# Kernel tuning notes

Hardware: AMD Instinct MI355X
Metric: run time of the kernel (lower is better)

Reference implementation:

```python
import jax, jax.numpy as jnp
import numpy as np

EPS = 1e-5


def _bn(h, gamma, beta):
    # BatchNorm1d in training mode: batch statistics over node dim
    mu = h.mean(axis=0)
    var = h.var(axis=0)
    return gamma * (h - mu) * jax.lax.rsqrt(var + EPS) + beta


def _rgcn_layer(x, src, dst, etype, W, Wloop, b, n_dst):
    # Relation-specific gather-transform-scatter (DGL RelGraphConv, sum agg,
    # self-loop + bias, no regularizer).
    x_src = x[src]                                   # [E, in] gather
    num_rels = W.shape[0]
    m = jnp.zeros((x_src.shape[0], W.shape[2]), x.dtype)
    for r in range(num_rels):                        # small fixed relation count
        m = m + jnp.where((etype == r)[:, None], x_src @ W[r], 0.0)
    agg = jax.ops.segment_sum(m, dst, num_segments=n_dst)  # scatter-add to dst
    # DGL block convention: dst nodes are the prefix of src nodes
    return agg + x[:n_dst] @ Wloop + b


def setup_inputs() -> dict:
    key = jax.random.key(0)
    ks = jax.random.split(key, 16)
    N_SRC, N_DST0, N_DST1 = 200000, 50000, 10000
    E0, E1, R, H, C = 800000, 160000, 5, 256, 153
    s = 1.0 / np.sqrt(H)
    inp = {
        "x": jax.random.normal(ks[0], (N_SRC, H), jnp.float32),
        "src0": jax.random.randint(ks[1], (E0,), 0, N_SRC, jnp.int32),
        "dst0": jax.random.randint(ks[2], (E0,), 0, N_DST0, jnp.int32),
        "etype0": jax.random.randint(ks[3], (E0,), 0, R, jnp.int32),
        "src1": jax.random.randint(ks[4], (E1,), 0, N_DST0, jnp.int32),
        "dst1": jax.random.randint(ks[5], (E1,), 0, N_DST1, jnp.int32),
        "etype1": jax.random.randint(ks[6], (E1,), 0, R, jnp.int32),
        "n_dst0": N_DST0,
        "n_dst1": N_DST1,
        "W0": jax.random.normal(ks[7], (R, H, H), jnp.float32) * s,
        "Wl0": jax.random.normal(ks[8], (H, H), jnp.float32) * s,
        "b0": jnp.zeros((H,), jnp.float32),
        "g0": jnp.ones((H,), jnp.float32),
        "be0": jnp.zeros((H,), jnp.float32),
        "W1": jax.random.normal(ks[9], (R, H, H), jnp.float32) * s,
        "Wl1": jax.random.normal(ks[10], (H, H), jnp.float32) * s,
        "b1": jnp.zeros((H,), jnp.float32),
        "g1": jnp.ones((H,), jnp.float32),
        "be1": jnp.zeros((H,), jnp.float32),
        "Wm1": jax.random.normal(ks[11], (H, H), jnp.float32) * s,
        "bm1": jnp.zeros((H,), jnp.float32),
        "gm": jnp.ones((H,), jnp.float32),
        "bem": jnp.zeros((H,), jnp.float32),
        "Wm2": jax.random.normal(ks[12], (H, C), jnp.float32) * s,
        "bm2": jnp.zeros((C,), jnp.float32),
    }
    return inp


def reference(x, src0, dst0, etype0, src1, dst1, etype1, n_dst0, n_dst1,
              W0, Wl0, b0, g0, be0, W1, Wl1, b1, g1, be1,
              Wm1, bm1, gm, bem, Wm2, bm2):
    # layer 0
    h = _rgcn_layer(x, src0, dst0, etype0, W0, Wl0, b0, n_dst0)
    h = jax.nn.elu(_bn(h, g0, be0))
    # layer 1
    h = _rgcn_layer(h, src1, dst1, etype1, W1, Wl1, b1, n_dst1)
    h = jax.nn.elu(_bn(h, g1, be1))
    # MLP head (dropout is identity in eval)
    h = jax.nn.relu(_bn(h @ Wm1 + bm1, gm, bem))
    return h @ Wm2 + bm2
```

## Files before the change

### kernel.cpp

```cpp
#include <hip/hip_runtime.h>
#include <hip/hip_bf16.h>


#define HD   256
#define EPS  1e-5f
#define NREL 5
#define ND0  50000
#define ND1  10000
#define BK   64
#define PAD  8

typedef unsigned short ushort_t;
using f32x4  = __attribute__((ext_vector_type(4))) float;
using short8 = __attribute__((ext_vector_type(8))) short;

__device__ __forceinline__ ushort_t f2b(float f) {
    union { float f; unsigned u; } x; x.f = f;
    unsigned r = x.u + 0x7FFF + ((x.u >> 16) & 1);
    return (ushort_t)(r >> 16);
}
__device__ __forceinline__ float b2f(ushort_t h) {
    union { unsigned u; float f; } x; x.u = ((unsigned)h) << 16;
    return x.f;
}

struct WconvArgs {
    const float* src[14];
    ushort_t*    dst[14];
    int          N[14];
};
__global__ void wconv_all_kernel(WconvArgs a) {
    int mat = blockIdx.x >> 8;
    int id = (blockIdx.x & 255) * 256 + threadIdx.x;
    int n = id >> 8, k = id & 255;
    int N = a.N[mat];
    float v = (n < N) ? a.src[mat][(size_t)k * N + n] : 0.f;
    a.dst[mat][id] = f2b(v);
}

__global__ void xconv_kernel(const float* __restrict__ x, ushort_t* __restrict__ xb,
                             int n4) {
    int id = blockIdx.x * 256 + threadIdx.x;
    if (id >= n4) return;
    float4 v = ((const float4*)x)[id];
    ushort4 o; o.x = f2b(v.x); o.y = f2b(v.y); o.z = f2b(v.z); o.w = f2b(v.w);
    ((ushort4*)xb)[id] = o;
}

__global__ void count2_kernel(const int* __restrict__ d0, const int* __restrict__ e0, int E0,
                              const int* __restrict__ d1, const int* __restrict__ e1, int E1,
                              int* __restrict__ cnt, int* __restrict__ pos) {
    int e = blockIdx.x * 256 + threadIdx.x;
    if (e < E0) {
        pos[e] = atomicAdd(&cnt[e0[e] * ND0 + d0[e]], 1);
    } else if (e < E0 + E1) {
        int i = e - E0;
        pos[e] = atomicAdd(&cnt[NREL * ND0 + e1[i] * ND1 + d1[i]], 1);
    }
}

__global__ void scan_block_kernel(const int* __restrict__ in, int* __restrict__ out,
                                  int* __restrict__ bsum, int nb) {
    __shared__ int ts[256];
    int tid = threadIdx.x;
    int base = blockIdx.x * 1024 + tid * 4;
    int v0 = (base + 0 < nb) ? in[base + 0] : 0;
    int v1 = (base + 1 < nb) ? in[base + 1] : 0;
    int v2 = (base + 2 < nb) ? in[base + 2] : 0;
    int v3 = (base + 3 < nb) ? in[base + 3] : 0;
    int tsum = v0 + v1 + v2 + v3;
    ts[tid] = tsum;
    __syncthreads();
    for (int d = 1; d < 256; d <<= 1) {
        int t = (tid >= d) ? ts[tid - d] : 0;
        __syncthreads();
        ts[tid] += t;
        __syncthreads();
    }
    int excl = ts[tid] - tsum;
    if (base + 0 < nb) out[base + 0] = excl;
    if (base + 1 < nb) out[base + 1] = excl + v0;
    if (base + 2 < nb) out[base + 2] = excl + v0 + v1;
    if (base + 3 < nb) out[base + 3] = excl + v0 + v1 + v2;
    if (tid == 255 && bsum) bsum[blockIdx.x] = ts[255];
}

__global__ void scan_add_kernel(int* __restrict__ out, const int* __restrict__ bsum, int nb) {
    int i = blockIdx.x * 256 + threadIdx.x;
    if (i < nb) out[i] += bsum[i >> 10];
}

__global__ void fill2_kernel(const int* __restrict__ s0, const int* __restrict__ d0,
                             const int* __restrict__ e0, int E0,
                             const int* __restrict__ s1, const int* __restrict__ d1,
                             const int* __restrict__ e1, int E1,
                             const int* __restrict__ pos, const int* __restrict__ off,
                             int* __restrict__ ssrc) {
    int e = blockIdx.x * 256 + threadIdx.x;
    if (e < E0) {
        ssrc[off[e0[e] * ND0 + d0[e]] + pos[e]] = s0[e];
    } else if (e < E0 + E1) {
        int i = e - E0;
        ssrc[off[NREL * ND0 + e1[i] * ND1 + d1[i]] + pos[e]] = s1[i];
    }
}

__global__ void gather_kernel(const ushort_t* __restrict__ feat, const int* __restrict__ ssrc,
                              const int* __restrict__ cnt, const int* __restrict__ off,
                              int nbuckets, ushort_t* __restrict__ out,
                              const float* __restrict__ sc, const float* __restrict__ sh) {
    int wave = (blockIdx.x * 256 + threadIdx.x) >> 6;
    int lane = threadIdx.x & 63;
    if (wave >= nbuckets) return;
    int deg = cnt[wave], s = off[wave];
    float4 scv = {0, 0, 0, 0}, shv = {0, 0, 0, 0};
    if (sc) { scv = ((const float4*)sc)[lane]; shv = ((const float4*)sh)[lane]; }
    float a0 = 0, a1 = 0, a2 = 0, a3 = 0;
    if (sc) {
        for (int j = 0; j < deg; j++) {
            ushort4 v = ((const ushort4*)(feat + (size_t)ssrc[s + j] * HD))[lane];
            float f0 = fmaf(b2f(v.x), scv.x, shv.x);
            float f1 = fmaf(b2f(v.y), scv.y, shv.y);
            float f2 = fmaf(b2f(v.z), scv.z, shv.z);
            float f3 = fmaf(b2f(v.w), scv.w, shv.w);
            a0 += f0 > 0.f ? f0 : expm1f(f0);
            a1 += f1 > 0.f ? f1 : expm1f(f1);
            a2 += f2 > 0.f ? f2 : expm1f(f2);
            a3 += f3 > 0.f ? f3 : expm1f(f3);
        }
    } else {
        int j = 0;
        for (; j + 2 <= deg; j += 2) {
            int r0 = ssrc[s + j], r1 = ssrc[s + j + 1];
            ushort4 v0 = ((const ushort4*)(feat + (size_t)r0 * HD))[lane];
            ushort4 v1 = ((const ushort4*)(feat + (size_t)r1 * HD))[lane];
            a0 += b2f(v0.x) + b2f(v1.x); a1 += b2f(v0.y) + b2f(v1.y);
            a2 += b2f(v0.z) + b2f(v1.z); a3 += b2f(v0.w) + b2f(v1.w);
        }
        if (j < deg) {
            ushort4 v = ((const ushort4*)(feat + (size_t)ssrc[s + j] * HD))[lane];
            a0 += b2f(v.x); a1 += b2f(v.y); a2 += b2f(v.z); a3 += b2f(v.w);
        }
    }
    ushort4 o; o.x = f2b(a0); o.y = f2b(a1); o.z = f2b(a2); o.w = f2b(a3);
    ((ushort4*)(out + (size_t)wave * HD))[lane] = o;
}

__global__ void bnprep_kernel(const float* __restrict__ sums, const float* __restrict__ g,
                              const float* __restrict__ be, float invM,
                              float* __restrict__ sc, float* __restrict__ sh) {
    int c = threadIdx.x;
    float mu = sums[c] * invM;
    float var = sums[HD + c] * invM - mu * mu;
    float s = g[c] * rsqrtf(var + EPS);
    sc[c] = s; sh[c] = be[c] - mu * s;
}

struct Seg {
    const ushort_t* A;
    const ushort_t* B;
    const float* sc;
    const float* sh;
    int act;
};
struct GemmArgs {
    Seg seg[6];
    int nseg;
    const float* bias;
    float* stats;
    ushort_t* Cb;
    float* Cf;
    int M, N;
};

template <int BM>
__launch_bounds__(256)
__global__ void gemm_mfma_kernel(GemmArgs g) {
    constexpr int F = BM / 32;
    __shared__ __align__(16) ushort_t As[BM][BK + PAD];
    __shared__ __align__(16) ushort_t Bs[BM][BK + PAD];
    int tid = threadIdx.x;
    int wave = tid >> 6, lane = tid & 63;
    int rq = lane >> 4, ci = lane & 15;
    int wm = (wave >> 1) * (BM / 2), wn = (wave & 1) * (BM / 2);
    int bm = blockIdx.y * BM, bn = blockIdx.x * BM;
    f32x4 acc[F][F] = {};
    int K = g.nseg * HD;

    for (int kk = 0; kk < K; kk += BK) {
        int si = kk >> 8;
        int kl = kk & 255;
        const ushort_t* Ap = g.seg[si].A;
        const ushort_t* Bp = g.seg[si].B;
        const float* sc = g.seg[si].sc;
#pragma unroll
        for (int it = 0; it < BM / 32; it++) {
            int idx = tid + it * 256;
            int row = idx >> 3, c8 = idx & 7;
            uint4 v = *(const uint4*)(Ap + (size_t)(bm + row) * HD + kl + c8 * 8);
            if (sc) {
                const float* sh = g.seg[si].sh;
                int act = g.seg[si].act;
                ushort_t* u = (ushort_t*)&v;
                int kb = kl + c8 * 8;
#pragma unroll
                for (int j = 0; j < 8; j++) {
                    float f = fmaf(b2f(u[j]), sc[kb + j], sh[kb + j]);
                    f = (act == 2) ? fmaxf(f, 0.f) : (f > 0.f ? f : expm1f(f));
                    u[j] = f2b(f);
                }
            }
            *(uint4*)&As[row][c8 * 8] = v;
        }
#pragma unroll
        for (int it = 0; it < BM / 32; it++) {
            int idx = tid + it * 256;
            int row = idx >> 3, c8 = idx & 7;
            *(uint4*)&Bs[row][c8 * 8] =
                *(const uint4*)(Bp + (size_t)(bn + row) * HD + kl + c8 * 8);
        }
        __syncthreads();
#pragma unroll
        for (int ks = 0; ks < BK; ks += 32) {
            int kq = ks + rq * 8;
            short8 a[F], b[F];
#pragma unroll
            for (int mi = 0; mi < F; mi++)
                a[mi] = *(const short8*)&As[wm + mi * 16 + ci][kq];
#pragma unroll
            for (int ni = 0; ni < F; ni++)
                b[ni] = *(const short8*)&Bs[wn + ni * 16 + ci][kq];
#pragma unroll
            for (int mi = 0; mi < F; mi++)
#pragma unroll
                for (int ni = 0; ni < F; ni++)
                    acc[mi][ni] = __builtin_amdgcn_mfma_f32_16x16x32_bf16(
                        a[mi], b[ni], acc[mi][ni], 0, 0, 0);
        }
        __syncthreads();
    }

#pragma unroll
    for (int ni = 0; ni < F; ni++) {
        int col = bn + wn + ni * 16 + ci;
        float bv = (col < g.N) ? g.bias[col] : 0.f;
#pragma unroll
        for (int mi = 0; mi < F; mi++)
#pragma unroll
            for (int reg = 0; reg < 4; reg++) acc[mi][ni][reg] += bv;
    }
    if (g.stats) {
#pragma unroll
        for (int ni = 0; ni < F; ni++) {
            float s = 0.f, s2 = 0.f;
#pragma unroll
            for (int mi = 0; mi < F; mi++)
#pragma unroll
                for (int reg = 0; reg < 4; reg++) {
                    int row = bm + wm + mi * 16 + rq * 4 + reg;
                    if (row < g.M) { float v = acc[mi][ni][reg]; s += v; s2 += v * v; }
                }
            s  += __shfl_xor(s, 16);  s  += __shfl_xor(s, 32);
            s2 += __shfl_xor(s2, 16); s2 += __shfl_xor(s2, 32);
            if (rq == 0) {
                int col = bn + wn + ni * 16 + ci;
                atomicAdd(&g.stats[col], s);
                atomicAdd(&g.stats[HD + col], s2);
            }
        }
    }
#pragma unroll
    for (int mi = 0; mi < F; mi++)
#pragma unroll
        for (int ni = 0; ni < F; ni++)
#pragma unroll
            for (int reg = 0; reg < 4; reg++) {
                int row = bm + wm + mi * 16 + rq * 4 + reg;
                int col = bn + wn + ni * 16 + ci;
                if (row < g.M && col < g.N) {
                    float v = acc[mi][ni][reg];
                    if (g.Cb) g.Cb[(size_t)row * HD + col] = f2b(v);
                    else      g.Cf[(size_t)row * g.N + col] = v;
                }
            }
}

extern "C" void kernel_launch(void* const* d_in, const int* in_sizes, int n_in,
                              void* d_out, int out_size, void* d_ws, size_t ws_size,
                              hipStream_t stream) {
    const float* x   = (const float*)d_in[0];
    const int* src0  = (const int*)d_in[1];
    const int* dst0  = (const int*)d_in[2];
    const int* et0   = (const int*)d_in[3];
    const int* src1  = (const int*)d_in[4];
    const int* dst1  = (const int*)d_in[5];
    const int* et1   = (const int*)d_in[6];
    const float* W0  = (const float*)d_in[9];
    const float* Wl0 = (const float*)d_in[10];
    const float* b0  = (const float*)d_in[11];
    const float* g0  = (const float*)d_in[12];
    const float* be0 = (const float*)d_in[13];
    const float* W1  = (const float*)d_in[14];
    const float* Wl1 = (const float*)d_in[15];
    const float* b1  = (const float*)d_in[16];
    const float* g1  = (const float*)d_in[17];
    const float* be1 = (const float*)d_in[18];
    const float* Wm1 = (const float*)d_in[19];
    const float* bm1 = (const float*)d_in[20];
    const float* gm  = (const float*)d_in[21];
    const float* bem = (const float*)d_in[22];
    const float* Wm2 = (const float*)d_in[23];
    const float* bm2 = (const float*)d_in[24];

    const int E0 = in_sizes[1];
    const int E1 = in_sizes[4];
    const int NOUT = in_sizes[24];
    const int NSRC = in_sizes[0] / HD;
    const int NBKT = NREL * ND0 + NREL * ND1;

    char* p = (char*)d_ws;
    ushort_t* Wt = (ushort_t*)p;  p += (size_t)14 * 65536 * 2;
    float* st    = (float*)p;     p += 1536 * 4;
    float* bnp   = (float*)p;     p += 6 * 256 * 4;
    int* cnt     = (int*)p;       p += (size_t)NBKT * 4;
    int* off     = (int*)p;       p += (size_t)NBKT * 4;
    int* bsum    = (int*)p;       p += 1024 * 4;
    int* pos     = (int*)p;       p += (size_t)(E0 + E1) * 4;
    int* ssrc    = (int*)p;       p += (size_t)(E0 + E1) * 4;
    ushort_t* xb  = (ushort_t*)p; p += (size_t)NSRC * HD * 2;
    ushort_t* S0  = (ushort_t*)p; p += (size_t)(NREL * ND0 + 128) * HD * 2;
    ushort_t* S1  = (ushort_t*)p; p += (size_t)(NREL * ND1 + 128) * HD * 2;
    ushort_t* h0b = (ushort_t*)p; p += (size_t)(ND0 + 128) * HD * 2;
    ushort_t* h1b = (ushort_t*)p; p += (size_t)(ND1 + 128) * HD * 2;
    ushort_t* mb  = (ushort_t*)p; p += (size_t)(ND1 + 128) * HD * 2;

    float* st0 = st, *st1 = st + 512, *stm = st + 1024;
    float* sc0 = bnp, *sh0 = bnp + 256, *sc1 = bnp + 512, *sh1 = bnp + 768;
    float* scm = bnp + 1024, *shm = bnp + 1280;

    ushort_t* W0t  = Wt;
    ushort_t* Wl0t = Wt + 5 * 65536;
    ushort_t* W1t  = Wt + 6 * 65536;
    ushort_t* Wl1t = Wt + 11 * 65536;
    ushort_t* Wm1t = Wt + 12 * 65536;
    ushort_t* Wm2t = Wt + 13 * 65536;

    {
        WconvArgs wa;
        for (int r = 0; r < NREL; r++) { wa.src[r] = W0 + (size_t)r * 65536; wa.dst[r] = W0t + (size_t)r * 65536; wa.N[r] = 256; }
        wa.src[5] = Wl0; wa.dst[5] = Wl0t; wa.N[5] = 256;
        for (int r = 0; r < NREL; r++) { wa.src[6 + r] = W1 + (size_t)r * 65536; wa.dst[6 + r] = W1t + (size_t)r * 65536; wa.N[6 + r] = 256; }
        wa.src[11] = Wl1; wa.dst[11] = Wl1t; wa.N[11] = 256;
        wa.src[12] = Wm1; wa.dst[12] = Wm1t; wa.N[12] = 256;
        wa.src[13] = Wm2; wa.dst[13] = Wm2t; wa.N[13] = NOUT;
        wconv_all_kernel<<<14 * 256, 256, 0, stream>>>(wa);
    }
    xconv_kernel<<<(NSRC * 64 + 255) / 256, 256, 0, stream>>>(x, xb, NSRC * 64);
    hipMemsetAsync(st, 0, 1536 * sizeof(float), stream);
    hipMemsetAsync(cnt, 0, (size_t)NBKT * sizeof(int), stream);

    int ET = E0 + E1;
    count2_kernel<<<(ET + 255) / 256, 256, 0, stream>>>(dst0, et0, E0, dst1, et1, E1, cnt, pos);
    int nsb = (NBKT + 1023) / 1024;
    scan_block_kernel<<<nsb, 256, 0, stream>>>(cnt, off, bsum, NBKT);
    scan_block_kernel<<<1, 256, 0, stream>>>(bsum, bsum, nullptr, nsb);
    scan_add_kernel<<<(NBKT + 255) / 256, 256, 0, stream>>>(off, bsum, NBKT);
    fill2_kernel<<<(ET + 255) / 256, 256, 0, stream>>>(src0, dst0, et0, E0, src1, dst1, et1, E1, pos, off, ssrc);

    gather_kernel<<<(NREL * ND0 * 64) / 256, 256, 0, stream>>>(
        xb, ssrc, cnt, off, NREL * ND0, S0, nullptr, nullptr);
    {
        GemmArgs ga = {};
        for (int s = 0; s < NREL; s++)
            ga.seg[s] = { S0 + (size_t)s * ND0 * HD, W0t + (size_t)s * 65536, nullptr, nullptr, 0 };
        ga.seg[5] = { xb, Wl0t, nullptr, nullptr, 0 };
        ga.nseg = 6; ga.bias = b0; ga.stats = st0;
        ga.Cb = h0b; ga.Cf = nullptr; ga.M = ND0; ga.N = HD;
        gemm_mfma_kernel<128><<<dim3(2, (ND0 + 127) / 128), 256, 0, stream>>>(ga);
    }
    bnprep_kernel<<<1, 256, 0, stream>>>(st0, g0, be0, 1.f / ND0, sc0, sh0);

    gather_kernel<<<(NREL * ND1 * 64) / 256, 256, 0, stream>>>(
        h0b, ssrc, cnt + NREL * ND0, off + NREL * ND0, NREL * ND1, S1, sc0, sh0);
    {
        GemmArgs ga = {};
        for (int s = 0; s < NREL; s++)
            ga.seg[s] = { S1 + (size_t)s * ND1 * HD, W1t + (size_t)s * 65536, nullptr, nullptr, 0 };
        ga.seg[5] = { h0b, Wl1t, sc0, sh0, 1 };
        ga.nseg = 6; ga.bias = b1; ga.stats = st1;
        ga.Cb = h1b; ga.Cf = nullptr; ga.M = ND1; ga.N = HD;
        gemm_mfma_kernel<64><<<dim3(4, (ND1 + 63) / 64), 256, 0, stream>>>(ga);
    }
    bnprep_kernel<<<1, 256, 0, stream>>>(st1, g1, be1, 1.f / ND1, sc1, sh1);

    {
        GemmArgs ga = {};
        ga.seg[0] = { h1b, Wm1t, sc1, sh1, 1 };
        ga.nseg = 1; ga.bias = bm1; ga.stats = stm;
        ga.Cb = mb; ga.Cf = nullptr; ga.M = ND1; ga.N = HD;
        gemm_mfma_kernel<64><<<dim3(4, (ND1 + 63) / 64), 256, 0, stream>>>(ga);
    }
    bnprep_kernel<<<1, 256, 0, stream>>>(stm, gm, bem, 1.f / ND1, scm, shm);
    {
        GemmArgs ga = {};
        ga.seg[0] = { mb, Wm2t, scm, shm, 2 };
        ga.nseg = 1; ga.bias = bm2; ga.stats = nullptr;
        ga.Cb = nullptr; ga.Cf = (float*)d_out; ga.M = ND1; ga.N = NOUT;
        gemm_mfma_kernel<64><<<dim3((NOUT + 63) / 64, (ND1 + 63) / 64), 256, 0, stream>>>(ga);
    }
}
```

Measured before the change: 820.7 us.

## Prefetch GEMM tiles into registers, swizzle LDS layout, unroll gather by four

The GEMM kernel now loads the next K tile from global memory into registers while MFMAs run on the current LDS tile, then writes it to shared memory after the compute. The padded shared-memory layout is replaced with an XOR swizzle to avoid bank conflicts at lower LDS usage, and launch bounds request two blocks per CU. The unnormalized gather loop is unrolled to four rows in flight to expose more memory parallelism. The register prefetch adds register pressure, which could clash with the occupancy hint.

```diff
diff --git a/kernel.cpp b/kernel.cpp
--- a/kernel.cpp
+++ b/kernel.cpp
@@ -8,7 +8,6 @@
 #define ND0  50000
 #define ND1  10000
 #define BK   64
-#define PAD  8
 
 typedef unsigned short ushort_t;
 using f32x4  = __attribute__((ext_vector_type(4))) float;
@@ -113,10 +112,10 @@
     int lane = threadIdx.x & 63;
     if (wave >= nbuckets) return;
     int deg = cnt[wave], s = off[wave];
-    float4 scv = {0, 0, 0, 0}, shv = {0, 0, 0, 0};
-    if (sc) { scv = ((const float4*)sc)[lane]; shv = ((const float4*)sh)[lane]; }
     float a0 = 0, a1 = 0, a2 = 0, a3 = 0;
     if (sc) {
+        float4 scv = ((const float4*)sc)[lane];
+        float4 shv = ((const float4*)sh)[lane];
         for (int j = 0; j < deg; j++) {
             ushort4 v = ((const ushort4*)(feat + (size_t)ssrc[s + j] * HD))[lane];
             float f0 = fmaf(b2f(v.x), scv.x, shv.x);
@@ -130,14 +129,19 @@
         }
     } else {
         int j = 0;
-        for (; j + 2 <= deg; j += 2) {
+        for (; j + 4 <= deg; j += 4) {
             int r0 = ssrc[s + j], r1 = ssrc[s + j + 1];
+            int r2 = ssrc[s + j + 2], r3 = ssrc[s + j + 3];
             ushort4 v0 = ((const ushort4*)(feat + (size_t)r0 * HD))[lane];
             ushort4 v1 = ((const ushort4*)(feat + (size_t)r1 * HD))[lane];
-            a0 += b2f(v0.x) + b2f(v1.x); a1 += b2f(v0.y) + b2f(v1.y);
-            a2 += b2f(v0.z) + b2f(v1.z); a3 += b2f(v0.w) + b2f(v1.w);
-        }
-        if (j < deg) {
+            ushort4 v2 = ((const ushort4*)(feat + (size_t)r2 * HD))[lane];
+            ushort4 v3 = ((const ushort4*)(feat + (size_t)r3 * HD))[lane];
+            a0 += (b2f(v0.x) + b2f(v1.x)) + (b2f(v2.x) + b2f(v3.x));
+            a1 += (b2f(v0.y) + b2f(v1.y)) + (b2f(v2.y) + b2f(v3.y));
+            a2 += (b2f(v0.z) + b2f(v1.z)) + (b2f(v2.z) + b2f(v3.z));
+            a3 += (b2f(v0.w) + b2f(v1.w)) + (b2f(v2.w) + b2f(v3.w));
+        }
+        for (; j < deg; j++) {
             ushort4 v = ((const ushort4*)(feat + (size_t)ssrc[s + j] * HD))[lane];
             a0 += b2f(v.x); a1 += b2f(v.y); a2 += b2f(v.z); a3 += b2f(v.w);
         }
@@ -174,11 +178,12 @@
 };
 
 template <int BM>
-__launch_bounds__(256)
+__launch_bounds__(256, 2)
 __global__ void gemm_mfma_kernel(GemmArgs g) {
-    constexpr int F = BM / 32;
-    __shared__ __align__(16) ushort_t As[BM][BK + PAD];
-    __shared__ __align__(16) ushort_t Bs[BM][BK + PAD];
+    constexpr int F  = BM / 32;
+    constexpr int IT = BM / 32;
+    __shared__ __align__(16) ushort_t As[BM * BK];
+    __shared__ __align__(16) ushort_t Bs[BM * BK];
     int tid = threadIdx.x;
     int wave = tid >> 6, lane = tid & 63;
     int rq = lane >> 4, ci = lane & 15;
@@ -187,22 +192,36 @@
     f32x4 acc[F][F] = {};
     int K = g.nseg * HD;
 
-    for (int kk = 0; kk < K; kk += BK) {
-        int si = kk >> 8;
-        int kl = kk & 255;
+    uint4 ra[IT], rb[IT];
+    int srow[IT], soct[IT];
+#pragma unroll
+    for (int it = 0; it < IT; it++) {
+        int idx = tid + it * 256;
+        srow[it] = idx >> 3;
+        soct[it] = idx & 7;
+    }
+
+    auto load_tile = [&](int kk) {
+        int si = kk >> 8, kl = kk & 255;
         const ushort_t* Ap = g.seg[si].A;
         const ushort_t* Bp = g.seg[si].B;
+#pragma unroll
+        for (int it = 0; it < IT; it++) {
+            ra[it] = *(const uint4*)(Ap + (size_t)(bm + srow[it]) * HD + kl + soct[it] * 8);
+            rb[it] = *(const uint4*)(Bp + (size_t)(bn + srow[it]) * HD + kl + soct[it] * 8);
+        }
+    };
+    auto store_tile = [&](int kk) {
+        int si = kk >> 8, kl = kk & 255;
         const float* sc = g.seg[si].sc;
 #pragma unroll
-        for (int it = 0; it < BM / 32; it++) {
-            int idx = tid + it * 256;
-            int row = idx >> 3, c8 = idx & 7;
-            uint4 v = *(const uint4*)(Ap + (size_t)(bm + row) * HD + kl + c8 * 8);
+        for (int it = 0; it < IT; it++) {
+            uint4 v = ra[it];
             if (sc) {
                 const float* sh = g.seg[si].sh;
                 int act = g.seg[si].act;
                 ushort_t* u = (ushort_t*)&v;
-                int kb = kl + c8 * 8;
+                int kb = kl + soct[it] * 8;
 #pragma unroll
                 for (int j = 0; j < 8; j++) {
                     float f = fmaf(b2f(u[j]), sc[kb + j], sh[kb + j]);
@@ -210,26 +229,31 @@
                     u[j] = f2b(f);
                 }
             }
-            *(uint4*)&As[row][c8 * 8] = v;
-        }
-#pragma unroll
-        for (int it = 0; it < BM / 32; it++) {
-            int idx = tid + it * 256;
-            int row = idx >> 3, c8 = idx & 7;
-            *(uint4*)&Bs[row][c8 * 8] =
-                *(const uint4*)(Bp + (size_t)(bn + row) * HD + kl + c8 * 8);
-        }
+            int sw = soct[it] ^ (srow[it] & 7);
+            *(uint4*)&As[srow[it] * BK + sw * 8] = v;
+            *(uint4*)&Bs[srow[it] * BK + sw * 8] = rb[it];
+        }
+    };
+
+    load_tile(0);
+    store_tile(0);
+    for (int kk = 0; kk < K; kk += BK) {
         __syncthreads();
+        if (kk + BK < K) load_tile(kk + BK);
 #pragma unroll
         for (int ks = 0; ks < BK; ks += 32) {
-            int kq = ks + rq * 8;
+            int O = (ks >> 3) + rq;
             short8 a[F], b[F];
 #pragma unroll
-            for (int mi = 0; mi < F; mi++)
-                a[mi] = *(const short8*)&As[wm + mi * 16 + ci][kq];
-#pragma unroll
-            for (int ni = 0; ni < F; ni++)
-                b[ni] = *(const short8*)&Bs[wn + ni * 16 + ci][kq];
+            for (int mi = 0; mi < F; mi++) {
+                int R = wm + mi * 16 + ci;
+                a[mi] = *(const short8*)&As[R * BK + ((O ^ (R & 7)) * 8)];
+            }
+#pragma unroll
+            for (int ni = 0; ni < F; ni++) {
+                int R = wn + ni * 16 + ci;
+                b[ni] = *(const short8*)&Bs[R * BK + ((O ^ (R & 7)) * 8)];
+            }
 #pragma unroll
             for (int mi = 0; mi < F; mi++)
 #pragma unroll
@@ -238,6 +262,7 @@
                         a[mi], b[ni], acc[mi][ni], 0, 0, 0);
         }
         __syncthreads();
+        if (kk + BK < K) store_tile(kk + BK);
     }
 
 #pragma unroll
```

After: 832.3 us. No clear change (+1.4%).

## Replace LDS-tiled GEMM with direct global-to-register MFMA loads; unroll gather by four

Applied to the files above, without the earlier changes.

The GEMM no longer stages A and B tiles through shared memory with barriers. Each wave instead loads its MFMA fragments straight from global memory into registers and relies on cache for reuse between waves, with an occupancy hint of 3 blocks per CU. The intent is to remove LDS traffic and __syncthreads stalls, at the risk of redundant global and L2 loads across waves and less coalesced access. Separately, the unnormalised gather loop is unrolled from two to four rows per iteration to keep more loads in flight.

```diff
diff --git a/kernel.cpp b/kernel.cpp
--- a/kernel.cpp
+++ b/kernel.cpp
@@ -7,8 +7,6 @@
 #define NREL 5
 #define ND0  50000
 #define ND1  10000
-#define BK   64
-#define PAD  8
 
 typedef unsigned short ushort_t;
 using f32x4  = __attribute__((ext_vector_type(4))) float;
@@ -113,10 +111,10 @@
     int lane = threadIdx.x & 63;
     if (wave >= nbuckets) return;
     int deg = cnt[wave], s = off[wave];
-    float4 scv = {0, 0, 0, 0}, shv = {0, 0, 0, 0};
-    if (sc) { scv = ((const float4*)sc)[lane]; shv = ((const float4*)sh)[lane]; }
     float a0 = 0, a1 = 0, a2 = 0, a3 = 0;
     if (sc) {
+        float4 scv = ((const float4*)sc)[lane];
+        float4 shv = ((const float4*)sh)[lane];
         for (int j = 0; j < deg; j++) {
             ushort4 v = ((const ushort4*)(feat + (size_t)ssrc[s + j] * HD))[lane];
             float f0 = fmaf(b2f(v.x), scv.x, shv.x);
@@ -130,14 +128,19 @@
         }
     } else {
         int j = 0;
-        for (; j + 2 <= deg; j += 2) {
+        for (; j + 4 <= deg; j += 4) {
             int r0 = ssrc[s + j], r1 = ssrc[s + j + 1];
+            int r2 = ssrc[s + j + 2], r3 = ssrc[s + j + 3];
             ushort4 v0 = ((const ushort4*)(feat + (size_t)r0 * HD))[lane];
             ushort4 v1 = ((const ushort4*)(feat + (size_t)r1 * HD))[lane];
-            a0 += b2f(v0.x) + b2f(v1.x); a1 += b2f(v0.y) + b2f(v1.y);
-            a2 += b2f(v0.z) + b2f(v1.z); a3 += b2f(v0.w) + b2f(v1.w);
+            ushort4 v2 = ((const ushort4*)(feat + (size_t)r2 * HD))[lane];
+            ushort4 v3 = ((const ushort4*)(feat + (size_t)r3 * HD))[lane];
+            a0 += (b2f(v0.x) + b2f(v1.x)) + (b2f(v2.x) + b2f(v3.x));
+            a1 += (b2f(v0.y) + b2f(v1.y)) + (b2f(v2.y) + b2f(v3.y));
+            a2 += (b2f(v0.z) + b2f(v1.z)) + (b2f(v2.z) + b2f(v3.z));
+            a3 += (b2f(v0.w) + b2f(v1.w)) + (b2f(v2.w) + b2f(v3.w));
         }
-        if (j < deg) {
+        for (; j < deg; j++) {
             ushort4 v = ((const ushort4*)(feat + (size_t)ssrc[s + j] * HD))[lane];
             a0 += b2f(v.x); a1 += b2f(v.y); a2 += b2f(v.z); a3 += b2f(v.w);
         }
@@ -173,71 +176,76 @@
     int M, N;
 };
 
-template <int BM>
-__launch_bounds__(256)
-__global__ void gemm_mfma_kernel(GemmArgs g) {
-    constexpr int F = BM / 32;
-    __shared__ __align__(16) ushort_t As[BM][BK + PAD];
-    __shared__ __align__(16) ushort_t Bs[BM][BK + PAD];
+template <int F>
+__launch_bounds__(256, 3)
+__global__ void gemm_direct_kernel(GemmArgs g) {
+    constexpr int WT = F * 16;
     int tid = threadIdx.x;
     int wave = tid >> 6, lane = tid & 63;
     int rq = lane >> 4, ci = lane & 15;
-    int wm = (wave >> 1) * (BM / 2), wn = (wave & 1) * (BM / 2);
-    int bm = blockIdx.y * BM, bn = blockIdx.x * BM;
+    int wm = (wave >> 1) * WT, wn = (wave & 1) * WT;
+    int bm = blockIdx.y * (2 * WT), bn = blockIdx.x * (2 * WT);
     f32x4 acc[F][F] = {};
-    int K = g.nseg * HD;
-
-    for (int kk = 0; kk < K; kk += BK) {
-        int si = kk >> 8;
-        int kl = kk & 255;
-        const ushort_t* Ap = g.seg[si].A;
-        const ushort_t* Bp = g.seg[si].B;
-        const float* sc = g.seg[si].sc;
-#pragma unroll
-        for (int it = 0; it < BM / 32; it++) {
-            int idx = tid + it * 256;
-            int row = idx >> 3, c8 = idx & 7;
-            uint4 v = *(const uint4*)(Ap + (size_t)(bm + row) * HD + kl + c8 * 8);
-            if (sc) {
-                const float* sh = g.seg[si].sh;
-                int act = g.seg[si].act;
-                ushort_t* u = (ushort_t*)&v;
-                int kb = kl + c8 * 8;
-#pragma unroll
-                for (int j = 0; j < 8; j++) {
-                    float f = fmaf(b2f(u[j]), sc[kb + j], sh[kb + j]);
-                    f = (act == 2) ? fmaxf(f, 0.f) : (f > 0.f ? f : expm1f(f));
-                    u[j] = f2b(f);
+
+    size_t aoff[F], boff[F];
+#pragma unroll
+    for (int mi = 0; mi < F; mi++)
+        aoff[mi] = (size_t)(bm + wm + mi * 16 + ci) * HD + rq * 8;
+#pragma unroll
+    for (int ni = 0; ni < F; ni++)
+        boff[ni] = (size_t)(bn + wn + ni * 16 + ci) * HD + rq * 8;
+
+    for (int s = 0; s < g.nseg; s++) {
+        const ushort_t* Ap = g.seg[s].A;
+        const ushort_t* Bp = g.seg[s].B;
+        const float* sc = g.seg[s].sc;
+        if (sc) {
+            const float* sh = g.seg[s].sh;
+            int act = g.seg[s].act;
+#pragma unroll 2
+            for (int kl = 0; kl < 256; kl += 32) {
+                short8 a[F], b[F];
+#pragma unroll
+                for (int mi = 0; mi < F; mi++) {
+                    short8 v = *(const short8*)(Ap + aoff[mi] + kl);
+                    ushort_t* u = (ushort_t*)&v;
+                    int kb = kl + rq * 8;
+#pragma unroll
+                    for (int j = 0; j < 8; j++) {
+                        float f = fmaf(b2f(u[j]), sc[kb + j], sh[kb + j]);
+                        f = (act == 2) ? fmaxf(f, 0.f) : (f > 0.f ? f : expm1f(f));
+                        u[j] = f2b(f);
+                    }
+                    a[mi] = v;
                 }
+#pragma unroll
+                for (int ni = 0; ni < F; ni++)
+                    b[ni] = *(const short8*)(Bp + boff[ni] + kl);
+#pragma unroll
+                for (int mi = 0; mi < F; mi++)
+#pragma unroll
+                    for (int ni = 0; ni < F; ni++)
+                        acc[mi][ni] = __builtin_amdgcn_mfma_f32_16x16x32_bf16(
+                            a[mi], b[ni], acc[mi][ni], 0, 0, 0);
             }
-            *(uint4*)&As[row][c8 * 8] = v;
+        } else {
+#pragma unroll 2
+            for (int kl = 0; kl < 256; kl += 32) {
+                short8 a[F], b[F];
+#pragma unroll
+                for (int mi = 0; mi < F; mi++)
+                    a[mi] = *(const short8*)(Ap + aoff[mi] + kl);
+#pragma unroll
+                for (int ni = 0; ni < F; ni++)
+                    b[ni] = *(const short8*)(Bp + boff[ni] + kl);
+#pragma unroll
+                for (int mi = 0; mi < F; mi++)
+#pragma unroll
+                    for (int ni = 0; ni < F; ni++)
+                        acc[mi][ni] = __builtin_amdgcn_mfma_f32_16x16x32_bf16(
+                            a[mi], b[ni], acc[mi][ni], 0, 0, 0);
+            }
         }
-#pragma unroll
-        for (int it = 0; it < BM / 32; it++) {
-            int idx = tid + it * 256;
-            int row = idx >> 3, c8 = idx & 7;
-            *(uint4*)&Bs[row][c8 * 8] =
-                *(const uint4*)(Bp + (size_t)(bn + row) * HD + kl + c8 * 8);
-        }
-        __syncthreads();
-#pragma unroll
-        for (int ks = 0; ks < BK; ks += 32) {
-            int kq = ks + rq * 8;
-            short8 a[F], b[F];
-#pragma unroll
-            for (int mi = 0; mi < F; mi++)
-                a[mi] = *(const short8*)&As[wm + mi * 16 + ci][kq];
-#pragma unroll
-            for (int ni = 0; ni < F; ni++)
-                b[ni] = *(const short8*)&Bs[wn + ni * 16 + ci][kq];
-#pragma unroll
-            for (int mi = 0; mi < F; mi++)
-#pragma unroll
-                for (int ni = 0; ni < F; ni++)
-                    acc[mi][ni] = __builtin_amdgcn_mfma_f32_16x16x32_bf16(
-                        a[mi], b[ni], acc[mi][ni], 0, 0, 0);
-        }
-        __syncthreads();
     }
 
 #pragma unroll
@@ -376,7 +384,7 @@
         ga.seg[5] = { xb, Wl0t, nullptr, nullptr, 0 };
         ga.nseg = 6; ga.bias = b0; ga.stats = st0;
         ga.Cb = h0b; ga.Cf = nullptr; ga.M = ND0; ga.N = HD;
-        gemm_mfma_kernel<128><<<dim3(2, (ND0 + 127) / 128), 256, 0, stream>>>(ga);
+        gemm_direct_kernel<4><<<dim3(2, (ND0 + 127) / 128), 256, 0, stream>>>(ga);
     }
     bnprep_kernel<<<1, 256, 0, stream>>>(st0, g0, be0, 1.f / ND0, sc0, sh0);
 
@@ -389,7 +397,7 @@
         ga.seg[5] = { h0b, Wl1t, sc0, sh0, 1 };
         ga.nseg = 6; ga.bias = b1; ga.stats = st1;
         ga.Cb = h1b; ga.Cf = nullptr; ga.M = ND1; ga.N = HD;
-        gemm_mfma_kernel<64><<<dim3(4, (ND1 + 63) / 64), 256, 0, stream>>>(ga);
+        gemm_direct_kernel<2><<<dim3(4, (ND1 + 63) / 64), 256, 0, stream>>>(ga);
     }
     bnprep_kernel<<<1, 256, 0, stream>>>(st1, g1, be1, 1.f / ND1, sc1, sh1);
 
@@ -398,7 +406,7 @@
         ga.seg[0] = { h1b, Wm1t, sc1, sh1, 1 };
         ga.nseg = 1; ga.bias = bm1; ga.stats = stm;
         ga.Cb = mb; ga.Cf = nullptr; ga.M = ND1; ga.N = HD;
-        gemm_mfma_kernel<64><<<dim3(4, (ND1 + 63) / 64), 256, 0, stream>>>(ga);
+        gemm_direct_kernel<2><<<dim3(4, (ND1 + 63) / 64), 256, 0, stream>>>(ga);
     }
     bnprep_kernel<<<1, 256, 0, stream>>>(stm, gm, bem, 1.f / ND1, scm, shm);
     {
@@ -406,6 +414,6 @@
         ga.seg[0] = { mb, Wm2t, scm, shm, 2 };
         ga.nseg = 1; ga.bias = bm2; ga.stats = nullptr;
         ga.Cb = nullptr; ga.Cf = (float*)d_out; ga.M = ND1; ga.N = NOUT;
-        gemm_mfma_kernel<64><<<dim3((NOUT + 63) / 64, (ND1 + 63) / 64), 256, 0, stream>>>(ga);
-    }
-}
+        gemm_direct_kernel<2><<<dim3((NOUT + 63) / 64, (ND1 + 63) / 64), 256, 0, stream>>>(ga);
+    }
+}
```

Measured after the change: 941.1 us. +14.7%, slower.
